# Kernel tuning notes

Measured on AMD Instinct MI355X. Metric: run time of the kernel, lower is better.

The kernel has to match this reference:

```python
import jax, jax.numpy as jnp
import numpy as np

N_ENT = 50000
N_REL = 200
N_EDGE = 1_000_000
D = 64


def setup_inputs() -> dict:
    key = jax.random.key(0)
    ks = jax.random.split(key, 12)
    src = jax.random.randint(ks[0], (N_EDGE,), 0, N_ENT)
    rel = jax.random.randint(ks[1], (N_EDGE,), 0, N_REL)
    dst = jax.random.randint(ks[2], (N_EDGE,), 0, N_ENT)
    triples = jnp.stack([src, rel, dst], axis=1).astype(jnp.int64)  # [E,3]
    s = 1.0 / np.sqrt(D)
    return {
        "emb_e": jax.random.normal(ks[3], (N_ENT, D), jnp.float32) * s,
        "re_att": jax.random.normal(ks[4], (N_REL,), jnp.float32) * 0.1,
        "W1": jax.random.normal(ks[5], (D, D), jnp.float32) * s,
        "W2": jax.random.normal(ks[6], (D, D), jnp.float32) * s,
        "W3": jax.random.normal(ks[7], (D, D), jnp.float32) * s,
        "u": jax.random.normal(ks[8], (3 * D,), jnp.float32) * s,
        "en_weight": jax.random.normal(ks[9], (D, D), jnp.float32) * s,
        "re_weight": jax.random.normal(ks[10], (D, D), jnp.float32) * s,
        "re_spec": jax.random.normal(ks[11], (D,), jnp.float32) * s,
        "triples": triples,
    }


def _forward(emb_e, re_att, W1, W2, W3, u, en_weight, re_weight, re_spec, triples):
    src = triples[:, 0]
    rel = triples[:, 1]
    dst = triples[:, 2]
    n = emb_e.shape[0]

    def wgc(x, W):
        # relation-weighted message passing: out[s] += w[r] * x[d]
        msg = jax.ops.segment_sum(x[dst] * re_att[rel][:, None], src, num_segments=n)
        return jnp.tanh((x + msg) @ W)

    x = wgc(emb_e, W1)
    x = wgc(x, W2)
    x = wgc(x, W3)

    # GAT-style edge scores: e = LeakyReLU(u . [W_en h_i ; W_re r_spec ; W_en h_j])
    d = x.shape[1]
    hs = x @ en_weight.T                       # [N,d] = (en_weight @ h)^T rows
    z_src = hs @ u[:d]                         # [N]
    z_dst = hs @ u[2 * d:]                     # [N]
    z_mid = u[d:2 * d] @ (re_weight @ re_spec)  # scalar, same for every edge
    scores = jax.nn.leaky_relu(z_src[src] + z_mid + z_dst[dst], 0.01)  # [E]

    # softmax normalized over ALL triples (global denominator, per source code)
    alpha = jax.nn.softmax(scores)

    # out[src] += alpha_e * x[dst]
    out = jax.ops.segment_sum(alpha[:, None] * x[dst], src, num_segments=n)
    return out


def reference(emb_e, re_att, W1, W2, W3, u, en_weight, re_weight, re_spec, triples):
    return _forward(emb_e, re_att, W1, W2, W3, u, en_weight, re_weight, re_spec, triples)
```

## Files before the change

### kernel.cpp

```cpp
#include <hip/hip_runtime.h>
#include <math.h>

#define N_ENT  50000
#define N_REL  200
#define N_EDGE 1000000
#define CHUNK  196
#define NCH    64
#define ECH2   15625
#define NPART  4
#define NRNG   12500

#define WS_ZSUM   128
#define WS_ZMID   192
#define WS_AV     256
#define WS_BV     512
#define WS_WT     0x00001000
#define WS_BSUM   0x00010000
#define WS_BBASE  0x00011000
#define WS_TOT    0x00040000
#define WS_OFFS   0x00080000
#define WS_ZSRC   0x000C0000
#define WS_ZDST   0x00100000
#define WS_SNODE  0x00140000
#define WS_SRCS   0x00180000
#define WS_EB     0x00380000
#define WS_EPK    0x00780000
#define WS_HIST   0x00B80000
#define WS_XB1    0x00B80000
#define WS_XB0    0x01200000

typedef __attribute__((ext_vector_type(8))) short s16x8;
typedef __attribute__((ext_vector_type(4))) float f32x4;

__device__ __forceinline__ float bflo(unsigned u) { return __uint_as_float(u << 16); }
__device__ __forceinline__ float bfhi(unsigned u) { return __uint_as_float(u & 0xffff0000u); }
__device__ __forceinline__ float bf2f(unsigned short u) {
  return __uint_as_float(((unsigned)u) << 16);
}
__device__ __forceinline__ unsigned short f2bf(float f) {
  unsigned u = __float_as_uint(f);
  unsigned r = ((u >> 16) & 1u) + 0x7fffu;
  return (unsigned short)((u + r) >> 16);
}
__device__ __forceinline__ float fast_tanh(float x) {
  float ex = __expf(2.f * x);
  return 1.f - __fdividef(2.f, ex + 1.f);
}
__device__ __forceinline__ void fma8(float* acc, float wt, uint4 q) {
  acc[0] += wt * bflo(q.x); acc[1] += wt * bfhi(q.x);
  acc[2] += wt * bflo(q.y); acc[3] += wt * bfhi(q.y);
  acc[4] += wt * bflo(q.z); acc[5] += wt * bfhi(q.z);
  acc[6] += wt * bflo(q.w); acc[7] += wt * bfhi(q.w);
}
__device__ __forceinline__ int tri_is64(const void* tri) {
  int z = ((const int*)tri)[2 * (threadIdx.x & 63) + 1];
  return __ballot(z == 0) == ~0ull;
}

__global__ void k_conv(const float* __restrict__ x, unsigned short* __restrict__ xb) {
  int i = blockIdx.x * blockDim.x + threadIdx.x;
  if (i >= N_ENT * 16) return;
  float4 v = ((const float4*)x)[i];
  ushort4 o;
  o.x = f2bf(v.x); o.y = f2bf(v.y); o.z = f2bf(v.z); o.w = f2bf(v.w);
  ((ushort4*)xb)[i] = o;
}

__global__ void k_decode(const void* tri, unsigned short* __restrict__ srcs,
                         unsigned* __restrict__ eb) {
  int is64 = tri_is64(tri);
  int stride = gridDim.x * blockDim.x;
  if (is64) {
    const long long* t = (const long long*)tri;
    for (int e = blockIdx.x * blockDim.x + threadIdx.x; e < N_EDGE; e += stride) {
      int s = (int)t[3 * e], r = (int)t[3 * e + 1], d = (int)t[3 * e + 2];
      srcs[e] = (unsigned short)s;
      eb[e] = ((unsigned)r << 16) | (unsigned)d;
    }
  } else {
    const int* t = (const int*)tri;
    for (int e = blockIdx.x * blockDim.x + threadIdx.x; e < N_EDGE; e += stride) {
      int s = t[3 * e], r = t[3 * e + 1], d = t[3 * e + 2];
      srcs[e] = (unsigned short)s;
      eb[e] = ((unsigned)r << 16) | (unsigned)d;
    }
  }
}

__global__ void __launch_bounds__(256) k_hist(const unsigned short* __restrict__ srcs,
                                              unsigned short* __restrict__ hist) {
  __shared__ unsigned h[NRNG];
  int c = blockIdx.x >> 2, x = blockIdx.x & 3;
  int lo = x * NRNG;
  for (int i = threadIdx.x; i < NRNG; i += 256) h[i] = 0u;
  __syncthreads();
  int e0 = c * ECH2, e1 = e0 + ECH2;
  for (int e = e0 + threadIdx.x; e < e1; e += 256) {
    int rel = (int)srcs[e] - lo;
    if ((unsigned)rel < NRNG) atomicAdd(&h[rel], 1u);
  }
  __syncthreads();
  for (int i = threadIdx.x; i < NRNG; i += 256)
    hist[c * N_ENT + lo + i] = (unsigned short)h[i];
}

__global__ void __launch_bounds__(256) k_scanH(unsigned short* __restrict__ hist,
                                               int* __restrict__ tot, int* __restrict__ bsum) {
  int t = threadIdx.x;
  int s = blockIdx.x * CHUNK + t;
  int run = 0;
  if (t < CHUNK && s < N_ENT) {
    for (int c = 0; c < NCH; c++) {
      int v = hist[c * N_ENT + s];
      hist[c * N_ENT + s] = (unsigned short)run;
      run += v;
    }
    tot[s] = run;
  }
  int v = run;
  for (int o = 32; o; o >>= 1) v += __shfl_down(v, o);
  __shared__ int sm[4];
  if ((t & 63) == 0) sm[t >> 6] = v;
  __syncthreads();
  if (t == 0) bsum[blockIdx.x] = sm[0] + sm[1] + sm[2] + sm[3];
}

__global__ void __launch_bounds__(256) k_scanBpre(
    const int* __restrict__ bsum, int* __restrict__ bbase, int* __restrict__ offs,
    double* zsum, const float* u, const float* enw, const float* rew, const float* rsp,
    float* av, float* bv, float* zmid,
    const float* W1, const float* W2, const float* W3, unsigned short* wt) {
  __shared__ int sm[256];
  int t = threadIdx.x;
  int v = bsum[t];
  sm[t] = v;
  __syncthreads();
  for (int d = 1; d < 256; d <<= 1) {
    int x = (t >= d) ? sm[t - d] : 0;
    __syncthreads();
    sm[t] += x;
    __syncthreads();
  }
  bbase[t] = sm[t] - v;
  if (t == 255) offs[N_ENT] = sm[255];
  if (t == 0) *zsum = 0.0;
  if (t < 64) {
    int k = t;
    float aa = 0.f, bb = 0.f;
    for (int j = 0; j < 64; j++) {
      float w = enw[j * 64 + k];
      aa += u[j] * w;
      bb += u[128 + j] * w;
    }
    av[k] = aa; bv[k] = bb;
    float z = 0.f;
    for (int c = 0; c < 64; c++) z += rew[k * 64 + c] * rsp[c];
    z *= u[64 + k];
    for (int o = 32; o; o >>= 1) z += __shfl_down(z, o);
    if (k == 0) *zmid = z;
  }
  for (int idx = t; idx < 4096; idx += 256) {
    int k = idx >> 6, n = idx & 63;
    wt[0 * 4608 + n * 72 + k] = f2bf(W1[idx]);
    wt[1 * 4608 + n * 72 + k] = f2bf(W2[idx]);
    wt[2 * 4608 + n * 72 + k] = f2bf(W3[idx]);
  }
}

__global__ void k_scanC(const int* __restrict__ counts, const int* __restrict__ bbase,
                        int* __restrict__ offs) {
  __shared__ int sm[256];
  int t = threadIdx.x;
  int i = blockIdx.x * CHUNK + t;
  int v = (t < CHUNK && i < N_ENT) ? counts[i] : 0;
  sm[t] = v;
  __syncthreads();
  for (int d = 1; d < 256; d <<= 1) {
    int x = (t >= d) ? sm[t - d] : 0;
    __syncthreads();
    sm[t] += x;
    __syncthreads();
  }
  if (t < CHUNK && i < N_ENT)
    offs[i] = bbase[blockIdx.x] + sm[t] - v;
}

__global__ void __launch_bounds__(256) k_scatter(
    const unsigned short* __restrict__ srcs, const unsigned* __restrict__ eb,
    const unsigned short* __restrict__ cbase, const int* __restrict__ offs,
    unsigned* __restrict__ epk) {
  __shared__ unsigned h[NRNG];
  int c = blockIdx.x >> 2, x = blockIdx.x & 3;
  int lo = x * NRNG;
  for (int i = threadIdx.x; i < NRNG; i += 256) h[i] = 0u;
  __syncthreads();
  int e0 = c * ECH2, e1 = e0 + ECH2;
  for (int e = e0 + threadIdx.x; e < e1; e += 256) {
    int s = (int)srcs[e];
    int rel = s - lo;
    if ((unsigned)rel < NRNG) {
      int lr = atomicAdd(&h[rel], 1u);
      epk[offs[s] + (int)cbase[c * N_ENT + s] + lr] = eb[e];
    }
  }
}

template <int EPI>
__global__ void __launch_bounds__(256) k_wgc(
    const unsigned short* __restrict__ xb, const unsigned short* __restrict__ wt,
    const int* __restrict__ offs, const unsigned* __restrict__ epk,
    const float* __restrict__ re_att, unsigned short* __restrict__ yb,
    const float* __restrict__ av, const float* __restrict__ bv,
    float* __restrict__ zsrc, float* __restrict__ zdst) {
  __shared__ __align__(16) unsigned short s_m[16 * 72];
  __shared__ __align__(16) unsigned short s_wt[64 * 72];
  __shared__ float s_att[N_REL];
  for (int i = threadIdx.x; i < N_REL; i += 256) s_att[i] = re_att[i];
  for (int i = threadIdx.x; i < 1152; i += 256)
    ((uint2*)s_wt)[i] = ((const uint2*)wt)[i];
  __syncthreads();

  int wv = threadIdx.x >> 6, lane = threadIdx.x & 63;
  int g = lane >> 3, c8 = (lane & 7) * 8;
  float fa = 0.f, fb = 0.f;
  if (EPI) { fa = av[lane]; fb = bv[lane]; }

  for (int i = 0; i < 4; i++) {
    int nl = wv * 4 + i;
    int node = blockIdx.x * 16 + nl;
    int e0 = offs[node], e1 = offs[node + 1];
    float acc[8] = {0.f, 0.f, 0.f, 0.f, 0.f, 0.f, 0.f, 0.f};
    {
      uint4 q = *(const uint4*)(xb + (size_t)node * 64 + c8);
      fma8(acc, (g == 0) ? 1.f : 0.f, q);
    }
    for (int e = e0; e < e1; e += 16) {
      int ia = e + g, ib = ia + 8;
      bool va = ia < e1, vb = ib < e1;
      unsigned pa = epk[va ? ia : e0];
      unsigned pb = epk[vb ? ib : e0];
      float wa = va ? s_att[pa >> 16] : 0.f;
      float wb = vb ? s_att[pb >> 16] : 0.f;
      unsigned ra = va ? (pa & 0xffffu) : 0u;
      unsigned rb = vb ? (pb & 0xffffu) : 0u;
      uint4 qa = *(const uint4*)(xb + (size_t)ra * 64 + c8);
      uint4 qb = *(const uint4*)(xb + (size_t)rb * 64 + c8);
      fma8(acc, wa, qa);
      fma8(acc, wb, qb);
    }
#pragma unroll
    for (int off = 8; off <= 32; off <<= 1)
#pragma unroll
      for (int c = 0; c < 8; c++) acc[c] += __shfl_xor(acc[c], off);
    if (lane < 8) {
      uint4 pk;
      pk.x = (unsigned)f2bf(acc[0]) | ((unsigned)f2bf(acc[1]) << 16);
      pk.y = (unsigned)f2bf(acc[2]) | ((unsigned)f2bf(acc[3]) << 16);
      pk.z = (unsigned)f2bf(acc[4]) | ((unsigned)f2bf(acc[5]) << 16);
      pk.w = (unsigned)f2bf(acc[6]) | ((unsigned)f2bf(acc[7]) << 16);
      *(uint4*)&s_m[nl * 72 + lane * 8] = pk;
    }
  }
  __syncthreads();

  int ar = (lane & 15) * 72 + (lane >> 4) * 8;
  int br = (wv * 16 + (lane & 15)) * 72 + (lane >> 4) * 8;
  s16x8 a0 = *(const s16x8*)&s_m[ar];
  s16x8 a1 = *(const s16x8*)&s_m[ar + 32];
  s16x8 b0 = *(const s16x8*)&s_wt[br];
  s16x8 b1 = *(const s16x8*)&s_wt[br + 32];
  f32x4 c = {0.f, 0.f, 0.f, 0.f};
  c = __builtin_amdgcn_mfma_f32_16x16x32_bf16(a0, b0, c, 0, 0, 0);
  c = __builtin_amdgcn_mfma_f32_16x16x32_bf16(a1, b1, c, 0, 0, 0);
  __syncthreads();
#pragma unroll
  for (int q = 0; q < 4; q++) {
    int r = (lane >> 4) * 4 + q;
    s_m[r * 72 + wv * 16 + (lane & 15)] = f2bf(fast_tanh(c[q]));
  }
  __syncthreads();

  {
    int r = threadIdx.x >> 4, c0 = (threadIdx.x & 15) * 4;
    ushort4 o;
    o.x = s_m[r * 72 + c0]; o.y = s_m[r * 72 + c0 + 1];
    o.z = s_m[r * 72 + c0 + 2]; o.w = s_m[r * 72 + c0 + 3];
    *(ushort4*)(yb + ((size_t)blockIdx.x * 16 + r) * 64 + c0) = o;
  }
  if (EPI) {
    for (int i = 0; i < 4; i++) {
      int nl = wv * 4 + i;
      float yf = bf2f(s_m[nl * 72 + lane]);
      float za = yf * fa, zb = yf * fb;
      for (int s = 32; s; s >>= 1) { za += __shfl_down(za, s); zb += __shfl_down(zb, s); }
      if (lane == 0) {
        int node = blockIdx.x * 16 + nl;
        zsrc[node] = za; zdst[node] = zb;
      }
    }
  }
}

__global__ void __launch_bounds__(256) k_out(
    const unsigned short* __restrict__ xb, const int* __restrict__ offs,
    const unsigned* __restrict__ epk, const float* __restrict__ zs,
    const float* __restrict__ zd, const float* zmid,
    float* __restrict__ out, float* __restrict__ snode) {
  int wid = (blockIdx.x * blockDim.x + threadIdx.x) >> 6;
  int lane = threadIdx.x & 63;
  if (wid >= N_ENT) return;
  int node = wid;
  int g = lane >> 3, c8 = (lane & 7) * 8;
  float zi = zs[node] + *zmid;
  float acc[8] = {0.f, 0.f, 0.f, 0.f, 0.f, 0.f, 0.f, 0.f};
  float s0 = 0.f;
  int e0 = offs[node], e1 = offs[node + 1];
  for (int e = e0; e < e1; e += 16) {
    int ia = e + g, ib = ia + 8;
    bool va = ia < e1, vb = ib < e1;
    unsigned pa = epk[va ? ia : e0];
    unsigned pb = epk[vb ? ib : e0];
    unsigned da = va ? (pa & 0xffffu) : 0u;
    unsigned db = vb ? (pb & 0xffffu) : 0u;
    float ca = zi + zd[da];
    float cb = zi + zd[db];
    ca = ca >= 0.f ? ca : 0.01f * ca;
    cb = cb >= 0.f ? cb : 0.01f * cb;
    float wa = va ? __expf(ca) : 0.f;
    float wb = vb ? __expf(cb) : 0.f;
    uint4 qa = *(const uint4*)(xb + (size_t)da * 64 + c8);
    uint4 qb = *(const uint4*)(xb + (size_t)db * 64 + c8);
    fma8(acc, wa, qa);
    fma8(acc, wb, qb);
    s0 += wa + wb;
  }
#pragma unroll
  for (int off = 8; off <= 32; off <<= 1) {
#pragma unroll
    for (int c = 0; c < 8; c++) acc[c] += __shfl_xor(acc[c], off);
    s0 += __shfl_xor(s0, off);
  }
  if (lane < 8) {
    float4* p = (float4*)(out + (size_t)node * 64 + lane * 8);
    p[0] = make_float4(acc[0], acc[1], acc[2], acc[3]);
    p[1] = make_float4(acc[4], acc[5], acc[6], acc[7]);
  }
  if (lane == 0) snode[node] = s0;
}

__global__ void k_red(const float* __restrict__ snode, double* zsum) {
  int stride = gridDim.x * blockDim.x;
  double s = 0.0;
  for (int i = blockIdx.x * blockDim.x + threadIdx.x; i < N_ENT; i += stride)
    s += (double)snode[i];
  for (int o = 32; o; o >>= 1) s += __shfl_down(s, o);
  __shared__ double ws_[4];
  if ((threadIdx.x & 63) == 0) ws_[threadIdx.x >> 6] = s;
  __syncthreads();
  if (threadIdx.x == 0)
    atomicAdd(zsum, ws_[0] + ws_[1] + ws_[2] + ws_[3]);
}

__global__ void k_norm(float* __restrict__ out, const double* zsum) {
  int i = blockIdx.x * blockDim.x + threadIdx.x;
  if (i >= N_ENT * 16) return;
  float invZ = (float)(1.0 / *zsum);
  float4 v = ((float4*)out)[i];
  v.x *= invZ; v.y *= invZ; v.z *= invZ; v.w *= invZ;
  ((float4*)out)[i] = v;
}

extern "C" void kernel_launch(void* const* d_in, const int* in_sizes, int n_in,
                              void* d_out, int out_size, void* d_ws, size_t ws_size,
                              hipStream_t stream) {
  const float* emb   = (const float*)d_in[0];
  const float* reatt = (const float*)d_in[1];
  const float* W1    = (const float*)d_in[2];
  const float* W2    = (const float*)d_in[3];
  const float* W3    = (const float*)d_in[4];
  const float* u     = (const float*)d_in[5];
  const float* enw   = (const float*)d_in[6];
  const float* rew   = (const float*)d_in[7];
  const float* rsp   = (const float*)d_in[8];
  const void*  tri   = d_in[9];

  char* ws = (char*)d_ws;
  double*         zsum   = (double*)(ws + WS_ZSUM);
  float*          zmid   = (float*)(ws + WS_ZMID);
  float*          av     = (float*)(ws + WS_AV);
  float*          bv     = (float*)(ws + WS_BV);
  unsigned short* wt     = (unsigned short*)(ws + WS_WT);
  int*            bsum   = (int*)(ws + WS_BSUM);
  int*            bbase  = (int*)(ws + WS_BBASE);
  int*            tot    = (int*)(ws + WS_TOT);
  int*            offs   = (int*)(ws + WS_OFFS);
  float*          zsrc   = (float*)(ws + WS_ZSRC);
  float*          zdst   = (float*)(ws + WS_ZDST);
  float*          snode  = (float*)(ws + WS_SNODE);
  unsigned short* srcs   = (unsigned short*)(ws + WS_SRCS);
  unsigned*       eb     = (unsigned*)(ws + WS_EB);
  unsigned*       epk    = (unsigned*)(ws + WS_EPK);
  unsigned short* hist   = (unsigned short*)(ws + WS_HIST);
  unsigned short* xb0    = (unsigned short*)(ws + WS_XB0);
  unsigned short* xb1    = (unsigned short*)(ws + WS_XB1);
  float*          out    = (float*)d_out;

  k_conv<<<3125, 256, 0, stream>>>(emb, xb0);
  k_decode<<<4096, 256, 0, stream>>>(tri, srcs, eb);
  k_hist<<<NCH * NPART, 256, 0, stream>>>(srcs, hist);
  k_scanH<<<256, 256, 0, stream>>>(hist, tot, bsum);
  k_scanBpre<<<1, 256, 0, stream>>>(bsum, bbase, offs, zsum, u, enw, rew, rsp,
                                    av, bv, zmid, W1, W2, W3, wt);
  k_scanC<<<256, 256, 0, stream>>>(tot, bbase, offs);
  k_scatter<<<NCH * NPART, 256, 0, stream>>>(srcs, eb, hist, offs, epk);

  k_wgc<0><<<3125, 256, 0, stream>>>(xb0, wt + 0 * 4608, offs, epk, reatt, xb1,
                                     nullptr, nullptr, nullptr, nullptr);
  k_wgc<0><<<3125, 256, 0, stream>>>(xb1, wt + 1 * 4608, offs, epk, reatt, xb0,
                                     nullptr, nullptr, nullptr, nullptr);
  k_wgc<1><<<3125, 256, 0, stream>>>(xb0, wt + 2 * 4608, offs, epk, reatt, xb1,
                                     av, bv, zsrc, zdst);

  k_out<<<12500, 256, 0, stream>>>(xb1, offs, epk, zsrc, zdst, zmid, out, snode);
  k_red<<<196, 256, 0, stream>>>(snode, zsum);
  k_norm<<<3125, 256, 0, stream>>>(out, zsum);
}
```

Before: 224.7 us.

## Pad per-node edge lists to multiples of 16 with dummy edges

Each node's CSR segment is rounded up to a multiple of 16 and filled with a dummy edge that points to a zero row (weight 0 in the conv, zd = -1e30 in the attention pass). This lets the inner gather loops drop their bounds checks and predicated selects. The cost is an extra fill kernel over a larger edge buffer, a workspace relayout, and extra gather traffic for padded slots; with about 20 edges per node, padding adds roughly half again as many entries.

```diff
diff --git a/kernel.cpp b/kernel.cpp
--- a/kernel.cpp
+++ b/kernel.cpp
@@ -9,6 +9,8 @@
 #define ECH2   15625
 #define NPART  4
 #define NRNG   12500
+#define EPK_CAP 1540096
+#define DUMMY  ((200u << 16) | 50000u)
 
 #define WS_ZSUM   128
 #define WS_ZMID   192
@@ -24,10 +26,10 @@
 #define WS_SNODE  0x00140000
 #define WS_SRCS   0x00180000
 #define WS_EB     0x00380000
-#define WS_EPK    0x00780000
-#define WS_HIST   0x00B80000
-#define WS_XB1    0x00B80000
-#define WS_XB0    0x01200000
+#define WS_XB0    0x00180000
+#define WS_EPK    0x007A0000
+#define WS_HIST   0x00D80000
+#define WS_XB1    0x00D80000
 
 typedef __attribute__((ext_vector_type(8))) short s16x8;
 typedef __attribute__((ext_vector_type(4))) float f32x4;
@@ -55,15 +57,6 @@
 __device__ __forceinline__ int tri_is64(const void* tri) {
   int z = ((const int*)tri)[2 * (threadIdx.x & 63) + 1];
   return __ballot(z == 0) == ~0ull;
-}
-
-__global__ void k_conv(const float* __restrict__ x, unsigned short* __restrict__ xb) {
-  int i = blockIdx.x * blockDim.x + threadIdx.x;
-  if (i >= N_ENT * 16) return;
-  float4 v = ((const float4*)x)[i];
-  ushort4 o;
-  o.x = f2bf(v.x); o.y = f2bf(v.y); o.z = f2bf(v.z); o.w = f2bf(v.w);
-  ((ushort4*)xb)[i] = o;
 }
 
 __global__ void k_decode(const void* tri, unsigned short* __restrict__ srcs,
@@ -108,16 +101,18 @@
                                                int* __restrict__ tot, int* __restrict__ bsum) {
   int t = threadIdx.x;
   int s = blockIdx.x * CHUNK + t;
-  int run = 0;
+  int padded = 0;
   if (t < CHUNK && s < N_ENT) {
+    int run = 0;
     for (int c = 0; c < NCH; c++) {
       int v = hist[c * N_ENT + s];
       hist[c * N_ENT + s] = (unsigned short)run;
       run += v;
     }
-    tot[s] = run;
-  }
-  int v = run;
+    padded = (run + 15) & ~15;
+    tot[s] = padded;
+  }
+  int v = padded;
   for (int o = 32; o; o >>= 1) v += __shfl_down(v, o);
   __shared__ int sm[4];
   if ((t & 63) == 0) sm[t >> 6] = v;
@@ -128,7 +123,7 @@
 __global__ void __launch_bounds__(256) k_scanBpre(
     const int* __restrict__ bsum, int* __restrict__ bbase, int* __restrict__ offs,
     double* zsum, const float* u, const float* enw, const float* rew, const float* rsp,
-    float* av, float* bv, float* zmid,
+    float* av, float* bv, float* zmid, float* zd,
     const float* W1, const float* W2, const float* W3, unsigned short* wt) {
   __shared__ int sm[256];
   int t = threadIdx.x;
@@ -144,6 +139,7 @@
   bbase[t] = sm[t] - v;
   if (t == 255) offs[N_ENT] = sm[255];
   if (t == 0) *zsum = 0.0;
+  if (t == 64) zd[N_ENT] = -1e30f;
   if (t < 64) {
     int k = t;
     float aa = 0.f, bb = 0.f;
@@ -183,6 +179,12 @@
   }
   if (t < CHUNK && i < N_ENT)
     offs[i] = bbase[blockIdx.x] + sm[t] - v;
+}
+
+__global__ void k_fill(unsigned* __restrict__ epk) {
+  int i = blockIdx.x * blockDim.x + threadIdx.x;
+  if (i * 4 < EPK_CAP)
+    ((uint4*)epk)[i] = make_uint4(DUMMY, DUMMY, DUMMY, DUMMY);
 }
 
 __global__ void __launch_bounds__(256) k_scatter(
@@ -202,6 +204,20 @@
       int lr = atomicAdd(&h[rel], 1u);
       epk[offs[s] + (int)cbase[c * N_ENT + s] + lr] = eb[e];
     }
+  }
+}
+
+__global__ void k_conv(const float* __restrict__ x, unsigned short* __restrict__ xb0,
+                       unsigned short* __restrict__ xb1) {
+  int i = blockIdx.x * blockDim.x + threadIdx.x;
+  if (i < N_ENT * 16) {
+    float4 v = ((const float4*)x)[i];
+    ushort4 o;
+    o.x = f2bf(v.x); o.y = f2bf(v.y); o.z = f2bf(v.z); o.w = f2bf(v.w);
+    ((ushort4*)xb0)[i] = o;
+  } else if (i < N_ENT * 16 + 16) {
+    ((ushort4*)xb0)[i] = make_ushort4(0, 0, 0, 0);
+    ((ushort4*)xb1)[i] = make_ushort4(0, 0, 0, 0);
   }
 }
 
@@ -214,8 +230,9 @@
     float* __restrict__ zsrc, float* __restrict__ zdst) {
   __shared__ __align__(16) unsigned short s_m[16 * 72];
   __shared__ __align__(16) unsigned short s_wt[64 * 72];
-  __shared__ float s_att[N_REL];
-  for (int i = threadIdx.x; i < N_REL; i += 256) s_att[i] = re_att[i];
+  __shared__ float s_att[N_REL + 1];
+  for (int i = threadIdx.x; i < N_REL + 1; i += 256)
+    s_att[i] = (i < N_REL) ? re_att[i] : 0.f;
   for (int i = threadIdx.x; i < 1152; i += 256)
     ((uint2*)s_wt)[i] = ((const uint2*)wt)[i];
   __syncthreads();
@@ -235,16 +252,12 @@
       fma8(acc, (g == 0) ? 1.f : 0.f, q);
     }
     for (int e = e0; e < e1; e += 16) {
-      int ia = e + g, ib = ia + 8;
-      bool va = ia < e1, vb = ib < e1;
-      unsigned pa = epk[va ? ia : e0];
-      unsigned pb = epk[vb ? ib : e0];
-      float wa = va ? s_att[pa >> 16] : 0.f;
-      float wb = vb ? s_att[pb >> 16] : 0.f;
-      unsigned ra = va ? (pa & 0xffffu) : 0u;
-      unsigned rb = vb ? (pb & 0xffffu) : 0u;
-      uint4 qa = *(const uint4*)(xb + (size_t)ra * 64 + c8);
-      uint4 qb = *(const uint4*)(xb + (size_t)rb * 64 + c8);
+      unsigned pa = epk[e + g];
+      unsigned pb = epk[e + g + 8];
+      float wa = s_att[pa >> 16];
+      float wb = s_att[pb >> 16];
+      uint4 qa = *(const uint4*)(xb + (size_t)(pa & 0xffffu) * 64 + c8);
+      uint4 qb = *(const uint4*)(xb + (size_t)(pb & 0xffffu) * 64 + c8);
       fma8(acc, wa, qa);
       fma8(acc, wb, qb);
     }
@@ -316,18 +329,16 @@
   float s0 = 0.f;
   int e0 = offs[node], e1 = offs[node + 1];
   for (int e = e0; e < e1; e += 16) {
-    int ia = e + g, ib = ia + 8;
-    bool va = ia < e1, vb = ib < e1;
-    unsigned pa = epk[va ? ia : e0];
-    unsigned pb = epk[vb ? ib : e0];
-    unsigned da = va ? (pa & 0xffffu) : 0u;
-    unsigned db = vb ? (pb & 0xffffu) : 0u;
+    unsigned pa = epk[e + g];
+    unsigned pb = epk[e + g + 8];
+    unsigned da = pa & 0xffffu;
+    unsigned db = pb & 0xffffu;
     float ca = zi + zd[da];
     float cb = zi + zd[db];
     ca = ca >= 0.f ? ca : 0.01f * ca;
     cb = cb >= 0.f ? cb : 0.01f * cb;
-    float wa = va ? __expf(ca) : 0.f;
-    float wb = vb ? __expf(cb) : 0.f;
+    float wa = __expf(ca);
+    float wb = __expf(cb);
     uint4 qa = *(const uint4*)(xb + (size_t)da * 64 + c8);
     uint4 qb = *(const uint4*)(xb + (size_t)db * 64 + c8);
     fma8(acc, wa, qa);
@@ -405,14 +416,15 @@
   unsigned short* xb1    = (unsigned short*)(ws + WS_XB1);
   float*          out    = (float*)d_out;
 
-  k_conv<<<3125, 256, 0, stream>>>(emb, xb0);
   k_decode<<<4096, 256, 0, stream>>>(tri, srcs, eb);
   k_hist<<<NCH * NPART, 256, 0, stream>>>(srcs, hist);
   k_scanH<<<256, 256, 0, stream>>>(hist, tot, bsum);
   k_scanBpre<<<1, 256, 0, stream>>>(bsum, bbase, offs, zsum, u, enw, rew, rsp,
-                                    av, bv, zmid, W1, W2, W3, wt);
+                                    av, bv, zmid, zdst, W1, W2, W3, wt);
   k_scanC<<<256, 256, 0, stream>>>(tot, bbase, offs);
+  k_fill<<<EPK_CAP / 1024, 256, 0, stream>>>(epk);
   k_scatter<<<NCH * NPART, 256, 0, stream>>>(srcs, eb, hist, offs, epk);
+  k_conv<<<3126, 256, 0, stream>>>(emb, xb0, xb1);
 
   k_wgc<0><<<3125, 256, 0, stream>>>(xb0, wt + 0 * 4608, offs, epk, reatt, xb1,
                                      nullptr, nullptr, nullptr, nullptr);
```

Result: no change. 224.7 us (+0.0%).
